# Kernel optimization log

Measured on AMD Instinct MI355X. Metric: run time of the kernel, lower is better.

## Reference

```python
import jax, jax.numpy as jnp
import numpy as np

C, R, T = 16, 1024, 4096
N = 500_000


def setup_inputs() -> dict:
    key = jax.random.key(0)
    k1, k2, k3 = jax.random.split(key, 3)
    rho = jax.random.randint(k1, (N,), 0, R, dtype=jnp.int32)
    theta = jax.random.randint(k2, (N,), 0, T, dtype=jnp.int32)
    f = jax.random.randint(k3, (N,), 0, C, dtype=jnp.int32)
    # buffers registered in __init__
    rp = jnp.arange(R + 1, dtype=jnp.float32)  # (R+1,)
    r = jnp.arange(R, dtype=jnp.float32)       # (R,)
    return {"rho": rho, "theta": theta, "f": f, "rp": rp, "r": r}


def reference(rho, theta, f, rp, r):
    # occ[f, rho, theta] = rho ; value stored equals its R-index, duplicates benign
    occ = jnp.full((C, R, T), -1, dtype=jnp.int32).at[f, rho, theta].set(rho)
    ids = jnp.argmax(occ, axis=1, keepdims=True)              # (C,1,T) largest occupied rho
    empty = jnp.all(occ == -1, axis=1, keepdims=True)         # no occupied point in column
    # torch uses ids=-1 -> rp[-1] == rp[R]; emulate wrap explicitly
    ids = jnp.where(empty, R, ids)
    return rp[ids] - r.reshape(1, -1, 1)                      # (C,R,T) float32
```

## Files before the change

kernel.cpp:

```cpp
#include <hip/hip_runtime.h>

#define C_DIM 16
#define R_DIM 1024
#define T_DIM 4096

typedef float f32x4 __attribute__((ext_vector_type(4)));


__global__ void scatter_max4(const int4* __restrict__ rho4,
                             const int4* __restrict__ theta4,
                             const int4* __restrict__ f4,
                             const int* __restrict__ rho,
                             const int* __restrict__ theta,
                             const int* __restrict__ f,
                             int* __restrict__ maxrho, int n) {
    int n4 = n >> 2;
    int i = blockIdx.x * blockDim.x + threadIdx.x;
    if (i < n4) {
        int4 rh = rho4[i], th = theta4[i], ff = f4[i];
        atomicMax(&maxrho[ff.x * T_DIM + th.x], rh.x);
        atomicMax(&maxrho[ff.y * T_DIM + th.y], rh.y);
        atomicMax(&maxrho[ff.z * T_DIM + th.z], rh.z);
        atomicMax(&maxrho[ff.w * T_DIM + th.w], rh.w);
    }
    if (i == 0) {
        for (int k = n4 << 2; k < n; ++k)
            atomicMax(&maxrho[f[k] * T_DIM + theta[k]], rho[k]);
    }
}

__global__ __launch_bounds__(256) void resolve_write(
        const int* __restrict__ maxrho,
        const float* __restrict__ rp,
        const float* __restrict__ r,
        float* __restrict__ out) {
    const int c   = blockIdx.x >> 5;
    const int t0  = ((blockIdx.x >> 3) & 3) * 1024;
    const int rr0 = (blockIdx.x & 7) * 128;

    const int4 m = *reinterpret_cast<const int4*>(
        maxrho + c * T_DIM + t0 + 4 * threadIdx.x);
    f32x4 v;
    v.x = rp[m.x < 0 ? R_DIM : m.x];
    v.y = rp[m.y < 0 ? R_DIM : m.y];
    v.z = rp[m.z < 0 ? R_DIM : m.z];
    v.w = rp[m.w < 0 ? R_DIM : m.w];

    float* base = out + ((size_t)(c * R_DIM + rr0)) * T_DIM + t0 + 4 * threadIdx.x;

#pragma unroll 4
    for (int j = 0; j < 128; ++j) {
        float rv = r[rr0 + j];
        f32x4 o = v - rv;
        __builtin_nontemporal_store(o, reinterpret_cast<f32x4*>(base + (size_t)j * T_DIM));
    }
}

extern "C" void kernel_launch(void* const* d_in, const int* in_sizes, int n_in,
                              void* d_out, int out_size, void* d_ws, size_t ws_size,
                              hipStream_t stream) {
    const int*   rho   = (const int*)d_in[0];
    const int*   theta = (const int*)d_in[1];
    const int*   f     = (const int*)d_in[2];
    const float* rp    = (const float*)d_in[3];
    const float* r     = (const float*)d_in[4];
    float* out = (float*)d_out;

    int* maxrho = (int*)d_ws;
    const int n = in_sizes[0];

    hipMemsetAsync(maxrho, 0xFF, (size_t)C_DIM * T_DIM * sizeof(int), stream);

    {
        int n4 = n >> 2;
        int blocks = (n4 + 255) / 256;
        scatter_max4<<<blocks, 256, 0, stream>>>(
            (const int4*)rho, (const int4*)theta, (const int4*)f,
            rho, theta, f, maxrho, n);
    }

    resolve_write<<<512, 256, 0, stream>>>(maxrho, rp, r, out);
}
```

Measured before the change: 74.21 us.

## Replicate scatter max table across blocks and merge replicas in resolve

Result: no change. 73.79 us (-0.6%).

```diff
diff --git a/kernel.cpp b/kernel.cpp
--- a/kernel.cpp
+++ b/kernel.cpp
@@ -3,43 +3,51 @@
 #define C_DIM 16
 #define R_DIM 1024
 #define T_DIM 4096
+#define TABLE (C_DIM * T_DIM)
+#define REP 8
 
 typedef float f32x4 __attribute__((ext_vector_type(4)));
 
 
-__global__ void scatter_max4(const int4* __restrict__ rho4,
-                             const int4* __restrict__ theta4,
-                             const int4* __restrict__ f4,
+__global__ void scatter_max2(const int2* __restrict__ rho2,
+                             const int2* __restrict__ theta2,
+                             const int2* __restrict__ f2,
                              const int* __restrict__ rho,
                              const int* __restrict__ theta,
                              const int* __restrict__ f,
-                             int* __restrict__ maxrho, int n) {
-    int n4 = n >> 2;
+                             int* __restrict__ maxrho,
+                             int rep_mask, int n) {
+    int* table = maxrho + (blockIdx.x & rep_mask) * TABLE;
+    int n2 = n >> 1;
     int i = blockIdx.x * blockDim.x + threadIdx.x;
-    if (i < n4) {
-        int4 rh = rho4[i], th = theta4[i], ff = f4[i];
-        atomicMax(&maxrho[ff.x * T_DIM + th.x], rh.x);
-        atomicMax(&maxrho[ff.y * T_DIM + th.y], rh.y);
-        atomicMax(&maxrho[ff.z * T_DIM + th.z], rh.z);
-        atomicMax(&maxrho[ff.w * T_DIM + th.w], rh.w);
+    if (i < n2) {
+        int2 rh = rho2[i], th = theta2[i], ff = f2[i];
+        atomicMax(&table[ff.x * T_DIM + th.x], rh.x);
+        atomicMax(&table[ff.y * T_DIM + th.y], rh.y);
     }
-    if (i == 0) {
-        for (int k = n4 << 2; k < n; ++k)
-            atomicMax(&maxrho[f[k] * T_DIM + theta[k]], rho[k]);
+    if (i == 0 && (n & 1)) {
+        int k = n - 1;
+        atomicMax(&table[f[k] * T_DIM + theta[k]], rho[k]);
     }
 }
 
 __global__ __launch_bounds__(256) void resolve_write(
-        const int* __restrict__ maxrho,
+        const int* __restrict__ maxrho, int rep,
         const float* __restrict__ rp,
         const float* __restrict__ r,
         float* __restrict__ out) {
     const int c   = blockIdx.x >> 5;
     const int t0  = ((blockIdx.x >> 3) & 3) * 1024;
     const int rr0 = (blockIdx.x & 7) * 128;
+    const int off = c * T_DIM + t0 + 4 * threadIdx.x;
 
-    const int4 m = *reinterpret_cast<const int4*>(
-        maxrho + c * T_DIM + t0 + 4 * threadIdx.x);
+    int4 m = *reinterpret_cast<const int4*>(maxrho + off);
+    for (int q = 1; q < rep; ++q) {
+        int4 mq = *reinterpret_cast<const int4*>(maxrho + q * TABLE + off);
+        m.x = max(m.x, mq.x); m.y = max(m.y, mq.y);
+        m.z = max(m.z, mq.z); m.w = max(m.w, mq.w);
+    }
+
     f32x4 v;
     v.x = rp[m.x < 0 ? R_DIM : m.x];
     v.y = rp[m.y < 0 ? R_DIM : m.y];
@@ -52,7 +60,7 @@
     for (int j = 0; j < 128; ++j) {
         float rv = r[rr0 + j];
         f32x4 o = v - rv;
-        __builtin_nontemporal_store(o, reinterpret_cast<f32x4*>(base + (size_t)j * T_DIM));
+        *reinterpret_cast<f32x4*>(base + (size_t)j * T_DIM) = o;
     }
 }
 
@@ -69,15 +77,17 @@
     int* maxrho = (int*)d_ws;
     const int n = in_sizes[0];
 
-    hipMemsetAsync(maxrho, 0xFF, (size_t)C_DIM * T_DIM * sizeof(int), stream);
+    const int rep = (ws_size >= (size_t)REP * TABLE * sizeof(int)) ? REP : 1;
+
+    hipMemsetAsync(maxrho, 0xFF, (size_t)rep * TABLE * sizeof(int), stream);
 
     {
-        int n4 = n >> 2;
-        int blocks = (n4 + 255) / 256;
-        scatter_max4<<<blocks, 256, 0, stream>>>(
-            (const int4*)rho, (const int4*)theta, (const int4*)f,
-            rho, theta, f, maxrho, n);
+        int n2 = n >> 1;
+        int blocks = (n2 + 255) / 256;
+        scatter_max2<<<blocks, 256, 0, stream>>>(
+            (const int2*)rho, (const int2*)theta, (const int2*)f,
+            rho, theta, f, maxrho, rep - 1, n);
     }
 
-    resolve_write<<<512, 256, 0, stream>>>(maxrho, rp, r, out);
+    resolve_write<<<512, 256, 0, stream>>>(maxrho, rep, rp, r, out);
 }
```
